# Performance work log

Hardware: AMD Instinct MI355X
Metric: run time of the kernel (lower is better)

Reference implementation:

```python
import jax, jax.numpy as jnp
import numpy as np

N = 100000      # nodes
E = 1600000     # directed edges (before self loops)
IN_DIM = 5
HID = 64
NEG_SLOPE = 0.2  # PyG GATConv default LeakyReLU slope


def setup_inputs() -> dict:
    key = jax.random.key(0)
    ks = jax.random.split(key, 12)
    x = jax.random.normal(ks[0], (N, IN_DIM), dtype=jnp.float32)
    edge_index = jax.random.randint(ks[1], (2, E), 0, N, dtype=jnp.int64)
    # layer 1 params (GATConv(5, HID), heads=1)
    W1 = jax.random.normal(ks[2], (IN_DIM, HID), dtype=jnp.float32) * (1.0 / np.sqrt(IN_DIM))
    a_src1 = jax.random.normal(ks[3], (HID,), dtype=jnp.float32) * 0.1
    a_dst1 = jax.random.normal(ks[4], (HID,), dtype=jnp.float32) * 0.1
    b1 = jnp.zeros((HID,), dtype=jnp.float32)
    # layer 2 params (GATConv(HID, 1))
    W2 = jax.random.normal(ks[5], (HID, 1), dtype=jnp.float32) * (1.0 / np.sqrt(HID))
    a_src2 = jax.random.normal(ks[6], (1,), dtype=jnp.float32) * 0.1
    a_dst2 = jax.random.normal(ks[7], (1,), dtype=jnp.float32) * 0.1
    b2 = jnp.zeros((1,), dtype=jnp.float32)
    return {"x": x, "edge_index": edge_index,
            "W1": W1, "a_src1": a_src1, "a_dst1": a_dst1, "b1": b1,
            "W2": W2, "a_src2": a_src2, "a_dst2": a_dst2, "b2": b2}


def _gat_layer(x, W, a_src, a_dst, b, src, dst):
    h = x @ W                                   # [N, F]
    s_src = h @ a_src                           # [N] per-node src score
    s_dst = h @ a_dst                           # [N] per-node dst score
    e = s_src[src] + s_dst[dst]                 # [E'] edge logits
    e = jnp.where(e > 0, e, NEG_SLOPE * e)      # LeakyReLU(0.2)
    # segment softmax over incoming edges of each dst node
    m = jax.ops.segment_max(e, dst, num_segments=N)
    ex = jnp.exp(e - m[dst])
    denom = jax.ops.segment_sum(ex, dst, num_segments=N)
    coef = ex / denom[dst]                      # [E'] attention coefficients
    out = jax.ops.segment_sum(coef[:, None] * h[src], dst, num_segments=N)
    return out + b


def reference(x, edge_index, W1, a_src1, a_dst1, b1, W2, a_src2, a_dst2, b2):
    si = jnp.arange(N, dtype=edge_index.dtype)  # add self loops (PyG default)
    src = jnp.concatenate([edge_index[0], si])
    dst = jnp.concatenate([edge_index[1], si])
    h = _gat_layer(x, W1, a_src1, a_dst1, b1, src, dst)
    h = jax.nn.relu(h)
    return _gat_layer(h, W2, a_src2, a_dst2, b2, src, dst)  # [N, 1]
```

## Files before the change

### kernel.cpp

```cpp
#include <hip/hip_runtime.h>
#include <hip/hip_bf16.h>
#include <hip/hip_fp16.h>

#define NN 100000
#define EE 1600000
#define ET (EE + NN)
#define HID 64
#define NEG 0.2f
#define NBUK 391
#define SCT_TILE 8192
#define BUKCAP 8192

__device__ __forceinline__ float uh(unsigned u) {
    __half_raw r; r.x = (unsigned short)(u & 0xFFFF);
    return __half2float(__half(r));
}
__device__ __forceinline__ unsigned f2h(float f) {
    __half h = __float2half_rn(f);
    __half_raw r = *reinterpret_cast<__half_raw*>(&h);
    return (unsigned)r.x;
}

#define NSCT ((ET + SCT_TILE - 1) / SCT_TILE)
#define NPROJB ((NN + 31) / 32)

__global__ __launch_bounds__(1024) void k_front(const float* __restrict__ x,
                                                const float* __restrict__ W1,
                                                const float* __restrict__ a_src1,
                                                const float* __restrict__ a_dst1,
                                                const int* __restrict__ ei,
                                                unsigned* __restrict__ rec,
                                                float* __restrict__ sd1,
                                                int* __restrict__ bcur,
                                                unsigned* __restrict__ pairs) {
    __shared__ unsigned sp[SCT_TILE];
    __shared__ unsigned short bid[SCT_TILE];
    __shared__ int cnt_[NBUK], loc[NBUK], cur[NBUK];
    __shared__ int wsum[16];
    int tid = threadIdx.x;

    if (blockIdx.x >= NSCT) {
        int p = blockIdx.x - NSCT;
        int wid  = tid >> 6;
        int half = (tid >> 5) & 1, li = tid & 31;
        int n = p * 32 + wid * 2 + half;
        if (n >= NN) return;
        float xv[5];
        float h0 = 0.f, h1 = 0.f;
#pragma unroll
        for (int k = 0; k < 5; ++k) {
            xv[k] = x[n * 5 + k];
            h0 += xv[k] * W1[k * HID + li];
            h1 += xv[k] * W1[k * HID + li + 32];
        }
        float a = h0 * a_src1[li] + h1 * a_src1[li + 32];
        float b = h0 * a_dst1[li] + h1 * a_dst1[li + 32];
#pragma unroll
        for (int o = 1; o <= 16; o <<= 1) { a += __shfl_xor(a, o); b += __shfl_xor(b, o); }
        if (li == 0) {
            sd1[n] = b;
            uint4 rv;
            rv.x = __float_as_uint(a);
            rv.y = f2h(xv[0]) | (f2h(xv[1]) << 16);
            rv.z = f2h(xv[2]) | (f2h(xv[3]) << 16);
            rv.w = f2h(xv[4]);
            *(uint4*)(rec + (size_t)n * 4) = rv;
        }
        return;
    }

    int wid = tid >> 6, lane = tid & 63;
    int base = blockIdx.x * SCT_TILE;
    int tilecnt = ET - base; if (tilecnt > SCT_TILE) tilecnt = SCT_TILE;

    for (int i = tid; i < NBUK; i += 1024) cnt_[i] = 0;
    __syncthreads();
    int sreg[8], dreg[8], rreg[8];
#pragma unroll
    for (int it = 0; it < 2; ++it) {
        int i = base + (it * 1024 + tid) * 4;
        if (i + 3 < EE) {
            const int4 sv = *(const int4*)(ei + i);
            const int4 dv = *(const int4*)(ei + EE + i);
            sreg[it*4+0] = sv.x; sreg[it*4+1] = sv.y; sreg[it*4+2] = sv.z; sreg[it*4+3] = sv.w;
            dreg[it*4+0] = dv.x; dreg[it*4+1] = dv.y; dreg[it*4+2] = dv.z; dreg[it*4+3] = dv.w;
        } else {
#pragma unroll
            for (int k = 0; k < 4; ++k) {
                int idx = i + k;
                if (idx < EE)      { sreg[it*4+k] = ei[idx];  dreg[it*4+k] = ei[EE + idx]; }
                else if (idx < ET) { sreg[it*4+k] = idx - EE; dreg[it*4+k] = idx - EE; }
                else               { dreg[it*4+k] = -1; }
            }
        }
#pragma unroll
        for (int k = 0; k < 4; ++k)
            if (dreg[it*4+k] >= 0) rreg[it*4+k] = atomicAdd(&cnt_[dreg[it*4+k] >> 8], 1);
    }
    __syncthreads();
    int b0 = tid * 4;
    int s0 = 0;
    if (b0 < NBUK)
        for (int k = 0; k < 4 && b0 + k < NBUK; ++k) s0 += cnt_[b0 + k];
    int incl = s0;
#pragma unroll
    for (int o = 1; o < 64; o <<= 1) {
        int t = __shfl(incl, (lane - o) & 63);
        if (lane >= o) incl += t;
    }
    if (lane == 63) wsum[wid] = incl;
    __syncthreads();
    int wpref = 0;
    for (int w = 0; w < wid; ++w) wpref += wsum[w];
    if (b0 < NBUK) {
        int run = wpref + incl - s0;
        for (int k = 0; k < 4 && b0 + k < NBUK; ++k) {
            loc[b0 + k] = run;
            run += cnt_[b0 + k];
        }
    }
    __syncthreads();
    for (int i = tid; i < NBUK; i += 1024) {
        int c = cnt_[i];
        cur[i] = c ? (atomicAdd(&bcur[i], c) + i * BUKCAP - loc[i]) : 0;
    }
    __syncthreads();
#pragma unroll
    for (int q = 0; q < 8; ++q) {
        if (dreg[q] >= 0) {
            int s = sreg[q], d = dreg[q];
            int b = d >> 8;
            int slot = loc[b] + rreg[q];
            sp[slot]  = ((unsigned)(d & 255) << 17) | (unsigned)s;
            bid[slot] = (unsigned short)b;
        }
    }
    __syncthreads();
    for (int i = tid; i < tilecnt; i += 1024)
        pairs[cur[bid[i]] + i] = sp[i];
}

__global__ __launch_bounds__(1024) void k_bsort(const int* __restrict__ bcur,
                                                unsigned* __restrict__ pairs,
                                                int2* __restrict__ rowcnt) {
    __shared__ int hist[256], sc[256];
    int b = blockIdx.x;
    int cnt = bcur[b];
    if (cnt > BUKCAP) cnt = BUKCAP;
    int base = b * BUKCAP;
    int tid = threadIdx.x;
    if (tid < 256) hist[tid] = 0;
    __syncthreads();
    unsigned preg[8];
    int rreg[8];
    int i0 = tid * 8;
    if (i0 + 8 <= cnt) {
        const uint4 v0 = *(const uint4*)(pairs + base + i0);
        const uint4 v1 = *(const uint4*)(pairs + base + i0 + 4);
        preg[0] = v0.x; preg[1] = v0.y; preg[2] = v0.z; preg[3] = v0.w;
        preg[4] = v1.x; preg[5] = v1.y; preg[6] = v1.z; preg[7] = v1.w;
    } else {
#pragma unroll
        for (int j = 0; j < 8; ++j)
            preg[j] = (i0 + j < cnt) ? pairs[base + i0 + j] : 0xFFFFFFFFu;
    }
#pragma unroll
    for (int j = 0; j < 8; ++j)
        if (preg[j] != 0xFFFFFFFFu) rreg[j] = atomicAdd(&hist[preg[j] >> 17], 1);
    __syncthreads();
    if (tid < 64) {
        int v0 = hist[4 * tid], v1 = hist[4 * tid + 1];
        int v2 = hist[4 * tid + 2], v3 = hist[4 * tid + 3];
        int s = v0 + v1 + v2 + v3;
#pragma unroll
        for (int o = 1; o < 64; o <<= 1) {
            int t = __shfl(s, (tid - o) & 63);
            if (tid >= o) s += t;
        }
        int excl = s - v0 - v1 - v2 - v3;
        sc[4 * tid]     = excl;
        sc[4 * tid + 1] = excl + v0;
        sc[4 * tid + 2] = excl + v0 + v1;
        sc[4 * tid + 3] = excl + v0 + v1 + v2;
    }
    __syncthreads();
    int nbase = b << 8;
    if (tid < 256 && nbase + tid < NN)
        rowcnt[nbase + tid] = make_int2(base + sc[tid], hist[tid]);
    int* adj = (int*)pairs;
#pragma unroll
    for (int j = 0; j < 8; ++j) {
        if (preg[j] != 0xFFFFFFFFu) {
            int ld = (int)(preg[j] >> 17);
            adj[base + sc[ld] + rreg[j]] = (int)(preg[j] & 0x1FFFF);
        }
    }
}

__device__ __forceinline__ void agg1_node_gen(int n, int lane, int off, int deg,
                                              const int* __restrict__ adj,
                                              const unsigned* __restrict__ rec,
                                              const float* __restrict__ sd1,
                                              const float* __restrict__ W1,
                                              const float* __restrict__ b1,
                                              const float* __restrict__ W2,
                                              float* __restrict__ h2) {
    float sdn = sd1[n];
    float dsum = 0.f, a0 = 0.f, a1 = 0.f, a2 = 0.f, a3 = 0.f, a4 = 0.f;
    for (int j0 = 0; j0 < deg; j0 += 64) {
        int j = j0 + lane;
        if (j < deg) {
            int s = adj[off + j];
            const uint4 v = *(const uint4*)(rec + (size_t)s * 4);
            float t = __uint_as_float(v.x) + sdn;
            float e = t > 0.f ? t : NEG * t;
            float w = __expf(e);
            dsum += w;
            a0 += w * uh(v.y); a1 += w * uh(v.y >> 16);
            a2 += w * uh(v.z); a3 += w * uh(v.z >> 16);
            a4 += w * uh(v.w);
        }
    }
#pragma unroll
    for (int o = 32; o; o >>= 1) {
        dsum += __shfl_xor(dsum, o);
        a0 += __shfl_xor(a0, o); a1 += __shfl_xor(a1, o); a2 += __shfl_xor(a2, o);
        a3 += __shfl_xor(a3, o); a4 += __shfl_xor(a4, o);
    }
    float inv = 1.0f / dsum;
    a0 *= inv; a1 *= inv; a2 *= inv; a3 *= inv; a4 *= inv;
    float of = b1[lane] + a0 * W1[lane] + a1 * W1[64 + lane] + a2 * W1[128 + lane]
             + a3 * W1[192 + lane] + a4 * W1[256 + lane];
    of = fmaxf(of, 0.f);
    float p2 = of * W2[lane];
#pragma unroll
    for (int o = 32; o; o >>= 1) p2 += __shfl_xor(p2, o);
    if (lane == 0) h2[n] = p2;
}

__global__ __launch_bounds__(256) void k_agg1(const int* __restrict__ rowcnt,
                                              const int* __restrict__ adj,
                                              const unsigned* __restrict__ rec,
                                              const float* __restrict__ sd1,
                                              const float* __restrict__ W1,
                                              const float* __restrict__ b1,
                                              const float* __restrict__ W2,
                                              float* __restrict__ h2) {
    int wid  = threadIdx.x >> 6;
    int lane = threadIdx.x & 63;
    int n0 = (blockIdx.x * 4 + wid) * 2;
    if (n0 >= NN) return;
    const int4 rc = *(const int4*)(rowcnt + n0 * 2);
    int off0 = rc.x, d0 = rc.y, off1 = rc.z, d1 = rc.w;

    if (d0 <= 32 && d1 <= 32) {
        int half = lane >> 5, li = lane & 31;
        int n = n0 + half;
        int off = half ? off1 : off0;
        int deg = half ? d1 : d0;
        float sdn = sd1[n];
        int s = adj[off + (li < deg ? li : 0)];
        const uint4 v = *(const uint4*)(rec + (size_t)s * 4);
        float t = __uint_as_float(v.x) + sdn;
        float e = t > 0.f ? t : NEG * t;
        float p = (li < deg) ? __expf(e) : 0.f;
        float ds = p;
        float a0 = p * uh(v.y), a1 = p * uh(v.y >> 16);
        float a2 = p * uh(v.z), a3 = p * uh(v.z >> 16);
        float a4 = p * uh(v.w);
#pragma unroll
        for (int o = 1; o <= 16; o <<= 1) {
            ds += __shfl_xor(ds, o);
            a0 += __shfl_xor(a0, o); a1 += __shfl_xor(a1, o); a2 += __shfl_xor(a2, o);
            a3 += __shfl_xor(a3, o); a4 += __shfl_xor(a4, o);
        }
        float inv = 1.0f / ds;
        a0 *= inv; a1 *= inv; a2 *= inv; a3 *= inv; a4 *= inv;
        float o0 = b1[li] + a0 * W1[li] + a1 * W1[64 + li] + a2 * W1[128 + li]
                 + a3 * W1[192 + li] + a4 * W1[256 + li];
        float o1 = b1[li + 32] + a0 * W1[li + 32] + a1 * W1[96 + li] + a2 * W1[160 + li]
                 + a3 * W1[224 + li] + a4 * W1[288 + li];
        o0 = fmaxf(o0, 0.f);
        o1 = fmaxf(o1, 0.f);
        float p2 = o0 * W2[li] + o1 * W2[li + 32];
#pragma unroll
        for (int o = 1; o <= 16; o <<= 1) p2 += __shfl_xor(p2, o);
        if (li == 0) h2[n] = p2;
    } else {
        agg1_node_gen(n0,     lane, off0, d0, adj, rec, sd1, W1, b1, W2, h2);
        agg1_node_gen(n0 + 1, lane, off1, d1, adj, rec, sd1, W1, b1, W2, h2);
    }
}

__device__ __forceinline__ void agg2_node(int n, int lane, int off, int deg,
                                          const int* __restrict__ adj,
                                          const float* __restrict__ h2,
                                          float as2v, float ad2v, float b2v,
                                          float* __restrict__ out) {
    float sdn = h2[n] * ad2v;
    float dsum = 0.f, nsum = 0.f;
    for (int j0 = 0; j0 < deg; j0 += 64) {
        int j = j0 + lane;
        if (j < deg) {
            int s = adj[off + j];
            float hv = h2[s];
            float e = hv * as2v + sdn;
            e = e > 0.f ? e : NEG * e;
            float ex = __expf(e);
            dsum += ex;
            nsum += ex * hv;
        }
    }
#pragma unroll
    for (int o = 32; o; o >>= 1) { dsum += __shfl_xor(dsum, o); nsum += __shfl_xor(nsum, o); }
    if (lane == 0) out[n] = nsum / dsum + b2v;
}

__global__ __launch_bounds__(256) void k_agg2(const int* __restrict__ rowcnt,
                                              const int* __restrict__ adj,
                                              const float* __restrict__ h2,
                                              const float* __restrict__ as2,
                                              const float* __restrict__ ad2,
                                              const float* __restrict__ b2,
                                              float* __restrict__ out) {
    int wid  = threadIdx.x >> 6;
    int lane = threadIdx.x & 63;
    int n0 = (blockIdx.x * 4 + wid) * 4;
    if (n0 >= NN) return;
    float as2v = as2[0], ad2v = ad2[0], b2v = b2[0];
    const int4 rcA = *(const int4*)(rowcnt + n0 * 2);
    const int4 rcB = *(const int4*)(rowcnt + n0 * 2 + 4);
    int d0 = rcA.y, d1 = rcA.w, d2 = rcB.y, d3 = rcB.w;

    if (d0 <= 32 && d1 <= 32 && d2 <= 32 && d3 <= 32) {
        int half = lane >> 5, li = lane & 31;
        int nA = n0 + half, nB = n0 + 2 + half;
        int offA = half ? rcA.z : rcA.x;
        int offB = half ? rcB.z : rcB.x;
        int degA = half ? d1 : d0, degB = half ? d3 : d2;
        float sdA = h2[nA] * ad2v, sdB = h2[nB] * ad2v;
        float hvA = 0.f, hvB = 0.f, pA = 0.f, pB = 0.f;
        if (li < degA) {
            hvA = h2[adj[offA + li]];
            float t = hvA * as2v + sdA;
            pA = __expf(t > 0.f ? t : NEG * t);
        }
        if (li < degB) {
            hvB = h2[adj[offB + li]];
            float t = hvB * as2v + sdB;
            pB = __expf(t > 0.f ? t : NEG * t);
        }
        float dsA = pA, dsB = pB, nsA = pA * hvA, nsB = pB * hvB;
#pragma unroll
        for (int o = 1; o <= 16; o <<= 1) {
            dsA += __shfl_xor(dsA, o); nsA += __shfl_xor(nsA, o);
            dsB += __shfl_xor(dsB, o); nsB += __shfl_xor(nsB, o);
        }
        if (li == 0) {
            out[nA] = nsA / dsA + b2v;
            out[nB] = nsB / dsB + b2v;
        }
    } else {
        agg2_node(n0,     lane, rcA.x, d0, adj, h2, as2v, ad2v, b2v, out);
        agg2_node(n0 + 1, lane, rcA.z, d1, adj, h2, as2v, ad2v, b2v, out);
        agg2_node(n0 + 2, lane, rcB.x, d2, adj, h2, as2v, ad2v, b2v, out);
        agg2_node(n0 + 3, lane, rcB.z, d3, adj, h2, as2v, ad2v, b2v, out);
    }
}

extern "C" void kernel_launch(void* const* d_in, const int* in_sizes, int n_in,
                              void* d_out, int out_size, void* d_ws, size_t ws_size,
                              hipStream_t stream) {
    const float* x      = (const float*)d_in[0];
    const int*   ei     = (const int*)d_in[1];
    const float* W1     = (const float*)d_in[2];
    const float* a_src1 = (const float*)d_in[3];
    const float* a_dst1 = (const float*)d_in[4];
    const float* b1     = (const float*)d_in[5];
    const float* W2     = (const float*)d_in[6];
    const float* as2    = (const float*)d_in[7];
    const float* ad2    = (const float*)d_in[8];
    const float* b2     = (const float*)d_in[9];
    float* out = (float*)d_out;

    unsigned* rec = (unsigned*)d_ws;
    float* sd1  = (float*)(rec + (size_t)NN * 4);
    float* h2   = sd1 + NN;
    int2* rowcnt = (int2*)(h2 + NN);
    int* bcur   = (int*)(rowcnt + NN);
    unsigned* pairs = (unsigned*)(bcur + 1024);
    int* adj    = (int*)pairs;

    const int NPAIR = (NN / 2 + 3) / 4;
    const int NQUAD = (NN + 15) / 16;

    hipMemsetAsync(bcur, 0, 1024 * sizeof(int), stream);
    k_front<<<NSCT + NPROJB, 1024, 0, stream>>>(x, W1, a_src1, a_dst1, ei,
                                                rec, sd1, bcur, pairs);
    k_bsort<<<NBUK, 1024, 0, stream>>>(bcur, pairs, rowcnt);
    k_agg1<<<NPAIR, 256, 0, stream>>>((const int*)rowcnt, adj, rec, sd1, W1, b1, W2, h2);
    k_agg2<<<NQUAD, 256, 0, stream>>>((const int*)rowcnt, adj, h2, as2, ad2, b2, out);
}
```

Before: 76.30 us.

## Fuse all GAT stages into one cooperative persistent kernel with grid syncs

Replaces the memset plus four kernel launches with a single cooperative persistent kernel. Blocks loop over work quanta for scatter and projection, bucket sort, layer-1 aggregation and layer-2 aggregation, separated by grid.sync. It also changes the bucket sort to stage the sorted adjacency in LDS and write it back contiguously. This targets launch gaps and inter-kernel drain at the cost of grid-wide barriers and a grid capped at 512 blocks of 1024 threads. The old multi-kernel path is kept as a fallback.

```diff
diff --git a/kernel.cpp b/kernel.cpp
--- a/kernel.cpp
+++ b/kernel.cpp
@@ -1,6 +1,9 @@
 #include <hip/hip_runtime.h>
 #include <hip/hip_bf16.h>
 #include <hip/hip_fp16.h>
+#include <hip/hip_cooperative_groups.h>
+
+namespace cg = cooperative_groups;
 
 #define NN 100000
 #define EE 1600000
@@ -10,6 +13,11 @@
 #define NBUK 391
 #define SCT_TILE 8192
 #define BUKCAP 8192
+#define TPB 1024
+#define NSCT ((ET + SCT_TILE - 1) / SCT_TILE)
+#define NPROJQ ((NN + 31) / 32)
+#define NAGG1Q ((NN + 31) / 32)
+#define NAGG2Q ((NN + 63) / 64)
 
 __device__ __forceinline__ float uh(unsigned u) {
     __half_raw r; r.x = (unsigned short)(u & 0xFFFF);
@@ -21,64 +29,20 @@
     return (unsigned)r.x;
 }
 
-#define NSCT ((ET + SCT_TILE - 1) / SCT_TILE)
-#define NPROJB ((NN + 31) / 32)
-
-__global__ __launch_bounds__(1024) void k_front(const float* __restrict__ x,
-                                                const float* __restrict__ W1,
-                                                const float* __restrict__ a_src1,
-                                                const float* __restrict__ a_dst1,
-                                                const int* __restrict__ ei,
-                                                unsigned* __restrict__ rec,
-                                                float* __restrict__ sd1,
-                                                int* __restrict__ bcur,
-                                                unsigned* __restrict__ pairs) {
-    __shared__ unsigned sp[SCT_TILE];
-    __shared__ unsigned short bid[SCT_TILE];
-    __shared__ int cnt_[NBUK], loc[NBUK], cur[NBUK];
-    __shared__ int wsum[16];
-    int tid = threadIdx.x;
-
-    if (blockIdx.x >= NSCT) {
-        int p = blockIdx.x - NSCT;
-        int wid  = tid >> 6;
-        int half = (tid >> 5) & 1, li = tid & 31;
-        int n = p * 32 + wid * 2 + half;
-        if (n >= NN) return;
-        float xv[5];
-        float h0 = 0.f, h1 = 0.f;
-#pragma unroll
-        for (int k = 0; k < 5; ++k) {
-            xv[k] = x[n * 5 + k];
-            h0 += xv[k] * W1[k * HID + li];
-            h1 += xv[k] * W1[k * HID + li + 32];
-        }
-        float a = h0 * a_src1[li] + h1 * a_src1[li + 32];
-        float b = h0 * a_dst1[li] + h1 * a_dst1[li + 32];
-#pragma unroll
-        for (int o = 1; o <= 16; o <<= 1) { a += __shfl_xor(a, o); b += __shfl_xor(b, o); }
-        if (li == 0) {
-            sd1[n] = b;
-            uint4 rv;
-            rv.x = __float_as_uint(a);
-            rv.y = f2h(xv[0]) | (f2h(xv[1]) << 16);
-            rv.z = f2h(xv[2]) | (f2h(xv[3]) << 16);
-            rv.w = f2h(xv[4]);
-            *(uint4*)(rec + (size_t)n * 4) = rv;
-        }
-        return;
-    }
-
-    int wid = tid >> 6, lane = tid & 63;
-    int base = blockIdx.x * SCT_TILE;
+
+template <typename SC>
+__device__ __forceinline__ void scatter_tile(SC& sc, int q, int tid, int wid, int lane,
+                                             const int* __restrict__ ei,
+                                             int* __restrict__ bcur,
+                                             unsigned* __restrict__ pairs) {
+    int base = q * SCT_TILE;
     int tilecnt = ET - base; if (tilecnt > SCT_TILE) tilecnt = SCT_TILE;
-
-    for (int i = tid; i < NBUK; i += 1024) cnt_[i] = 0;
+    for (int i = tid; i < NBUK; i += TPB) sc.cnt_[i] = 0;
     __syncthreads();
     int sreg[8], dreg[8], rreg[8];
 #pragma unroll
     for (int it = 0; it < 2; ++it) {
-        int i = base + (it * 1024 + tid) * 4;
+        int i = base + (it * TPB + tid) * 4;
         if (i + 3 < EE) {
             const int4 sv = *(const int4*)(ei + i);
             const int4 dv = *(const int4*)(ei + EE + i);
@@ -95,61 +59,94 @@
         }
 #pragma unroll
         for (int k = 0; k < 4; ++k)
-            if (dreg[it*4+k] >= 0) rreg[it*4+k] = atomicAdd(&cnt_[dreg[it*4+k] >> 8], 1);
+            if (dreg[it*4+k] >= 0) rreg[it*4+k] = atomicAdd(&sc.cnt_[dreg[it*4+k] >> 8], 1);
     }
     __syncthreads();
     int b0 = tid * 4;
     int s0 = 0;
     if (b0 < NBUK)
-        for (int k = 0; k < 4 && b0 + k < NBUK; ++k) s0 += cnt_[b0 + k];
+        for (int k = 0; k < 4 && b0 + k < NBUK; ++k) s0 += sc.cnt_[b0 + k];
     int incl = s0;
 #pragma unroll
     for (int o = 1; o < 64; o <<= 1) {
         int t = __shfl(incl, (lane - o) & 63);
         if (lane >= o) incl += t;
     }
-    if (lane == 63) wsum[wid] = incl;
+    if (lane == 63) sc.wsum[wid] = incl;
     __syncthreads();
     int wpref = 0;
-    for (int w = 0; w < wid; ++w) wpref += wsum[w];
+    for (int w = 0; w < wid; ++w) wpref += sc.wsum[w];
     if (b0 < NBUK) {
         int run = wpref + incl - s0;
         for (int k = 0; k < 4 && b0 + k < NBUK; ++k) {
-            loc[b0 + k] = run;
-            run += cnt_[b0 + k];
-        }
-    }
-    __syncthreads();
-    for (int i = tid; i < NBUK; i += 1024) {
-        int c = cnt_[i];
-        cur[i] = c ? (atomicAdd(&bcur[i], c) + i * BUKCAP - loc[i]) : 0;
-    }
-    __syncthreads();
-#pragma unroll
-    for (int q = 0; q < 8; ++q) {
-        if (dreg[q] >= 0) {
-            int s = sreg[q], d = dreg[q];
+            sc.loc[b0 + k] = run;
+            run += sc.cnt_[b0 + k];
+        }
+    }
+    __syncthreads();
+    for (int i = tid; i < NBUK; i += TPB) {
+        int c = sc.cnt_[i];
+        sc.cur[i] = c ? (atomicAdd(&bcur[i], c) + i * BUKCAP - sc.loc[i]) : 0;
+    }
+    __syncthreads();
+#pragma unroll
+    for (int p = 0; p < 8; ++p) {
+        if (dreg[p] >= 0) {
+            int s = sreg[p], d = dreg[p];
             int b = d >> 8;
-            int slot = loc[b] + rreg[q];
-            sp[slot]  = ((unsigned)(d & 255) << 17) | (unsigned)s;
-            bid[slot] = (unsigned short)b;
-        }
-    }
-    __syncthreads();
-    for (int i = tid; i < tilecnt; i += 1024)
-        pairs[cur[bid[i]] + i] = sp[i];
-}
-
-__global__ __launch_bounds__(1024) void k_bsort(const int* __restrict__ bcur,
-                                                unsigned* __restrict__ pairs,
-                                                int2* __restrict__ rowcnt) {
-    __shared__ int hist[256], sc[256];
-    int b = blockIdx.x;
+            int slot = sc.loc[b] + rreg[p];
+            sc.sp[slot]  = ((unsigned)(d & 255) << 17) | (unsigned)s;
+            sc.bid[slot] = (unsigned short)b;
+        }
+    }
+    __syncthreads();
+    for (int i = tid; i < tilecnt; i += TPB)
+        pairs[sc.cur[sc.bid[i]] + i] = sc.sp[i];
+    __syncthreads();
+}
+
+__device__ __forceinline__ void proj_quantum(int p, int tid, int wid,
+                                             const float* __restrict__ x,
+                                             const float* __restrict__ W1,
+                                             const float* __restrict__ a_src1,
+                                             const float* __restrict__ a_dst1,
+                                             unsigned* __restrict__ rec,
+                                             float* __restrict__ sd1) {
+    int half = (tid >> 5) & 1, li = tid & 31;
+    int n = p * 32 + wid * 2 + half;
+    if (n >= NN) return;
+    float xv[5];
+    float h0 = 0.f, h1 = 0.f;
+#pragma unroll
+    for (int k = 0; k < 5; ++k) {
+        xv[k] = x[n * 5 + k];
+        h0 += xv[k] * W1[k * HID + li];
+        h1 += xv[k] * W1[k * HID + li + 32];
+    }
+    float a = h0 * a_src1[li] + h1 * a_src1[li + 32];
+    float b = h0 * a_dst1[li] + h1 * a_dst1[li + 32];
+#pragma unroll
+    for (int o = 1; o <= 16; o <<= 1) { a += __shfl_xor(a, o); b += __shfl_xor(b, o); }
+    if (li == 0) {
+        sd1[n] = b;
+        uint4 rv;
+        rv.x = __float_as_uint(a);
+        rv.y = f2h(xv[0]) | (f2h(xv[1]) << 16);
+        rv.z = f2h(xv[2]) | (f2h(xv[3]) << 16);
+        rv.w = f2h(xv[4]);
+        *(uint4*)(rec + (size_t)n * 4) = rv;
+    }
+}
+
+template <typename BS>
+__device__ __forceinline__ void bsort_bucket(BS& bs, int b, int tid,
+                                             const int* __restrict__ bcur,
+                                             unsigned* __restrict__ pairs,
+                                             int2* __restrict__ rowcnt) {
     int cnt = bcur[b];
     if (cnt > BUKCAP) cnt = BUKCAP;
     int base = b * BUKCAP;
-    int tid = threadIdx.x;
-    if (tid < 256) hist[tid] = 0;
+    if (tid < 256) bs.hist[tid] = 0;
     __syncthreads();
     unsigned preg[8];
     int rreg[8];
@@ -166,11 +163,11 @@
     }
 #pragma unroll
     for (int j = 0; j < 8; ++j)
-        if (preg[j] != 0xFFFFFFFFu) rreg[j] = atomicAdd(&hist[preg[j] >> 17], 1);
+        if (preg[j] != 0xFFFFFFFFu) rreg[j] = atomicAdd(&bs.hist[preg[j] >> 17], 1);
     __syncthreads();
     if (tid < 64) {
-        int v0 = hist[4 * tid], v1 = hist[4 * tid + 1];
-        int v2 = hist[4 * tid + 2], v3 = hist[4 * tid + 3];
+        int v0 = bs.hist[4 * tid], v1 = bs.hist[4 * tid + 1];
+        int v2 = bs.hist[4 * tid + 2], v3 = bs.hist[4 * tid + 3];
         int s = v0 + v1 + v2 + v3;
 #pragma unroll
         for (int o = 1; o < 64; o <<= 1) {
@@ -178,81 +175,38 @@
             if (tid >= o) s += t;
         }
         int excl = s - v0 - v1 - v2 - v3;
-        sc[4 * tid]     = excl;
-        sc[4 * tid + 1] = excl + v0;
-        sc[4 * tid + 2] = excl + v0 + v1;
-        sc[4 * tid + 3] = excl + v0 + v1 + v2;
+        bs.scn[4 * tid]     = excl;
+        bs.scn[4 * tid + 1] = excl + v0;
+        bs.scn[4 * tid + 2] = excl + v0 + v1;
+        bs.scn[4 * tid + 3] = excl + v0 + v1 + v2;
     }
     __syncthreads();
     int nbase = b << 8;
     if (tid < 256 && nbase + tid < NN)
-        rowcnt[nbase + tid] = make_int2(base + sc[tid], hist[tid]);
-    int* adj = (int*)pairs;
+        rowcnt[nbase + tid] = make_int2(base + bs.scn[tid], bs.hist[tid]);
 #pragma unroll
     for (int j = 0; j < 8; ++j) {
         if (preg[j] != 0xFFFFFFFFu) {
             int ld = (int)(preg[j] >> 17);
-            adj[base + sc[ld] + rreg[j]] = (int)(preg[j] & 0x1FFFF);
-        }
-    }
-}
-
-__device__ __forceinline__ void agg1_node_gen(int n, int lane, int off, int deg,
-                                              const int* __restrict__ adj,
-                                              const unsigned* __restrict__ rec,
-                                              const float* __restrict__ sd1,
-                                              const float* __restrict__ W1,
-                                              const float* __restrict__ b1,
-                                              const float* __restrict__ W2,
-                                              float* __restrict__ h2) {
-    float sdn = sd1[n];
-    float dsum = 0.f, a0 = 0.f, a1 = 0.f, a2 = 0.f, a3 = 0.f, a4 = 0.f;
-    for (int j0 = 0; j0 < deg; j0 += 64) {
-        int j = j0 + lane;
-        if (j < deg) {
-            int s = adj[off + j];
-            const uint4 v = *(const uint4*)(rec + (size_t)s * 4);
-            float t = __uint_as_float(v.x) + sdn;
-            float e = t > 0.f ? t : NEG * t;
-            float w = __expf(e);
-            dsum += w;
-            a0 += w * uh(v.y); a1 += w * uh(v.y >> 16);
-            a2 += w * uh(v.z); a3 += w * uh(v.z >> 16);
-            a4 += w * uh(v.w);
-        }
-    }
-#pragma unroll
-    for (int o = 32; o; o >>= 1) {
-        dsum += __shfl_xor(dsum, o);
-        a0 += __shfl_xor(a0, o); a1 += __shfl_xor(a1, o); a2 += __shfl_xor(a2, o);
-        a3 += __shfl_xor(a3, o); a4 += __shfl_xor(a4, o);
-    }
-    float inv = 1.0f / dsum;
-    a0 *= inv; a1 *= inv; a2 *= inv; a3 *= inv; a4 *= inv;
-    float of = b1[lane] + a0 * W1[lane] + a1 * W1[64 + lane] + a2 * W1[128 + lane]
-             + a3 * W1[192 + lane] + a4 * W1[256 + lane];
-    of = fmaxf(of, 0.f);
-    float p2 = of * W2[lane];
-#pragma unroll
-    for (int o = 32; o; o >>= 1) p2 += __shfl_xor(p2, o);
-    if (lane == 0) h2[n] = p2;
-}
-
-__global__ __launch_bounds__(256) void k_agg1(const int* __restrict__ rowcnt,
-                                              const int* __restrict__ adj,
-                                              const unsigned* __restrict__ rec,
-                                              const float* __restrict__ sd1,
-                                              const float* __restrict__ W1,
-                                              const float* __restrict__ b1,
-                                              const float* __restrict__ W2,
-                                              float* __restrict__ h2) {
-    int wid  = threadIdx.x >> 6;
-    int lane = threadIdx.x & 63;
-    int n0 = (blockIdx.x * 4 + wid) * 2;
-    if (n0 >= NN) return;
-    const int4 rc = *(const int4*)(rowcnt + n0 * 2);
+            bs.srt[bs.scn[ld] + rreg[j]] = (int)(preg[j] & 0x1FFFF);
+        }
+    }
+    __syncthreads();
+    int* adj = (int*)pairs;
+    for (int i = tid; i < cnt; i += TPB)
+        adj[base + i] = bs.srt[i];
+    __syncthreads();
+}
+
+__device__ __forceinline__ void agg1_pair(int n0, int lane, const int4 rc,
+                                          const int* __restrict__ adj,
+                                          const unsigned* __restrict__ rec,
+                                          const float* __restrict__ sd1,
+                                          const float* __restrict__ W1,
+                                          const float* __restrict__ b1,
+                                          const float* __restrict__ W2,
+                                          float* __restrict__ h2) {
     int off0 = rc.x, d0 = rc.y, off1 = rc.z, d1 = rc.w;
-
     if (d0 <= 32 && d1 <= 32) {
         int half = lane >> 5, li = lane & 31;
         int n = n0 + half;
@@ -287,51 +241,51 @@
         for (int o = 1; o <= 16; o <<= 1) p2 += __shfl_xor(p2, o);
         if (li == 0) h2[n] = p2;
     } else {
-        agg1_node_gen(n0,     lane, off0, d0, adj, rec, sd1, W1, b1, W2, h2);
-        agg1_node_gen(n0 + 1, lane, off1, d1, adj, rec, sd1, W1, b1, W2, h2);
-    }
-}
-
-__device__ __forceinline__ void agg2_node(int n, int lane, int off, int deg,
+        for (int w = 0; w < 2; ++w) {
+            int n = n0 + w;
+            int off = w ? rc.z : rc.x;
+            int deg = w ? rc.w : rc.y;
+            float sdn = sd1[n];
+            float dsum = 0.f, a0 = 0.f, a1 = 0.f, a2 = 0.f, a3 = 0.f, a4 = 0.f;
+            for (int j0 = 0; j0 < deg; j0 += 64) {
+                int j = j0 + lane;
+                if (j < deg) {
+                    int s = adj[off + j];
+                    const uint4 v = *(const uint4*)(rec + (size_t)s * 4);
+                    float t = __uint_as_float(v.x) + sdn;
+                    float e = t > 0.f ? t : NEG * t;
+                    float ww = __expf(e);
+                    dsum += ww;
+                    a0 += ww * uh(v.y); a1 += ww * uh(v.y >> 16);
+                    a2 += ww * uh(v.z); a3 += ww * uh(v.z >> 16);
+                    a4 += ww * uh(v.w);
+                }
+            }
+#pragma unroll
+            for (int o = 32; o; o >>= 1) {
+                dsum += __shfl_xor(dsum, o);
+                a0 += __shfl_xor(a0, o); a1 += __shfl_xor(a1, o); a2 += __shfl_xor(a2, o);
+                a3 += __shfl_xor(a3, o); a4 += __shfl_xor(a4, o);
+            }
+            float inv = 1.0f / dsum;
+            a0 *= inv; a1 *= inv; a2 *= inv; a3 *= inv; a4 *= inv;
+            float of = b1[lane] + a0 * W1[lane] + a1 * W1[64 + lane] + a2 * W1[128 + lane]
+                     + a3 * W1[192 + lane] + a4 * W1[256 + lane];
+            of = fmaxf(of, 0.f);
+            float p2 = of * W2[lane];
+#pragma unroll
+            for (int o = 32; o; o >>= 1) p2 += __shfl_xor(p2, o);
+            if (lane == 0) h2[n] = p2;
+        }
+    }
+}
+
+__device__ __forceinline__ void agg2_quad(int n0, int lane, const int4 rcA, const int4 rcB,
                                           const int* __restrict__ adj,
                                           const float* __restrict__ h2,
                                           float as2v, float ad2v, float b2v,
                                           float* __restrict__ out) {
-    float sdn = h2[n] * ad2v;
-    float dsum = 0.f, nsum = 0.f;
-    for (int j0 = 0; j0 < deg; j0 += 64) {
-        int j = j0 + lane;
-        if (j < deg) {
-            int s = adj[off + j];
-            float hv = h2[s];
-            float e = hv * as2v + sdn;
-            e = e > 0.f ? e : NEG * e;
-            float ex = __expf(e);
-            dsum += ex;
-            nsum += ex * hv;
-        }
-    }
-#pragma unroll
-    for (int o = 32; o; o >>= 1) { dsum += __shfl_xor(dsum, o); nsum += __shfl_xor(nsum, o); }
-    if (lane == 0) out[n] = nsum / dsum + b2v;
-}
-
-__global__ __launch_bounds__(256) void k_agg2(const int* __restrict__ rowcnt,
-                                              const int* __restrict__ adj,
-                                              const float* __restrict__ h2,
-                                              const float* __restrict__ as2,
-                                              const float* __restrict__ ad2,
-                                              const float* __restrict__ b2,
-                                              float* __restrict__ out) {
-    int wid  = threadIdx.x >> 6;
-    int lane = threadIdx.x & 63;
-    int n0 = (blockIdx.x * 4 + wid) * 4;
-    if (n0 >= NN) return;
-    float as2v = as2[0], ad2v = ad2[0], b2v = b2[0];
-    const int4 rcA = *(const int4*)(rowcnt + n0 * 2);
-    const int4 rcB = *(const int4*)(rowcnt + n0 * 2 + 4);
     int d0 = rcA.y, d1 = rcA.w, d2 = rcB.y, d3 = rcB.w;
-
     if (d0 <= 32 && d1 <= 32 && d2 <= 32 && d3 <= 32) {
         int half = lane >> 5, li = lane & 31;
         int nA = n0 + half, nB = n0 + 2 + half;
@@ -361,11 +315,159 @@
             out[nB] = nsB / dsB + b2v;
         }
     } else {
-        agg2_node(n0,     lane, rcA.x, d0, adj, h2, as2v, ad2v, b2v, out);
-        agg2_node(n0 + 1, lane, rcA.z, d1, adj, h2, as2v, ad2v, b2v, out);
-        agg2_node(n0 + 2, lane, rcB.x, d2, adj, h2, as2v, ad2v, b2v, out);
-        agg2_node(n0 + 3, lane, rcB.z, d3, adj, h2, as2v, ad2v, b2v, out);
-    }
+        for (int w = 0; w < 4; ++w) {
+            int n = n0 + w;
+            int off = (w == 0) ? rcA.x : (w == 1) ? rcA.z : (w == 2) ? rcB.x : rcB.z;
+            int deg = (w == 0) ? d0 : (w == 1) ? d1 : (w == 2) ? d2 : d3;
+            float sdn = h2[n] * ad2v;
+            float dsum = 0.f, nsum = 0.f;
+            for (int j0 = 0; j0 < deg; j0 += 64) {
+                int j = j0 + lane;
+                if (j < deg) {
+                    int s = adj[off + j];
+                    float hv = h2[s];
+                    float e = hv * as2v + sdn;
+                    e = e > 0.f ? e : NEG * e;
+                    float ex = __expf(e);
+                    dsum += ex;
+                    nsum += ex * hv;
+                }
+            }
+#pragma unroll
+            for (int o = 32; o; o >>= 1) { dsum += __shfl_xor(dsum, o); nsum += __shfl_xor(nsum, o); }
+            if (lane == 0) out[n] = nsum / dsum + b2v;
+        }
+    }
+}
+
+struct ScatterLDS {
+    unsigned sp[SCT_TILE];
+    unsigned short bid[SCT_TILE];
+    int cnt_[NBUK], loc[NBUK], cur[NBUK];
+    int wsum[16];
+};
+struct BsortLDS {
+    int srt[BUKCAP];
+    int hist[256], scn[256];
+};
+
+__global__ __launch_bounds__(TPB, 2) void k_mega(const float* __restrict__ x,
+                                                 const float* __restrict__ W1,
+                                                 const float* __restrict__ a_src1,
+                                                 const float* __restrict__ a_dst1,
+                                                 const int* __restrict__ ei,
+                                                 const float* __restrict__ b1,
+                                                 const float* __restrict__ W2,
+                                                 const float* __restrict__ as2,
+                                                 const float* __restrict__ ad2,
+                                                 const float* __restrict__ b2,
+                                                 unsigned* __restrict__ rec,
+                                                 float* __restrict__ sd1,
+                                                 int* __restrict__ bcur,
+                                                 unsigned* __restrict__ pairs,
+                                                 int2* __restrict__ rowcnt,
+                                                 float* __restrict__ h2,
+                                                 float* __restrict__ out) {
+    cg::grid_group grid = cg::this_grid();
+    __shared__ union { ScatterLDS sc; BsortLDS bs; } sh;
+    int tid = threadIdx.x;
+    int wid = tid >> 6, lane = tid & 63;
+    int bx = blockIdx.x;
+    int GS = gridDim.x;
+    int* adj = (int*)pairs;
+
+    for (int i = bx * TPB + tid; i < 1024; i += GS * TPB) bcur[i] = 0;
+    grid.sync();
+
+    for (int q = bx; q < NSCT + NPROJQ; q += GS) {
+        if (q < NSCT)
+            scatter_tile(sh.sc, q, tid, wid, lane, ei, bcur, pairs);
+        else
+            proj_quantum(q - NSCT, tid, wid, x, W1, a_src1, a_dst1, rec, sd1);
+    }
+    grid.sync();
+
+    for (int b = bx; b < NBUK; b += GS)
+        bsort_bucket(sh.bs, b, tid, bcur, pairs, rowcnt);
+    grid.sync();
+
+    const int* rc32 = (const int*)rowcnt;
+    for (int q = bx; q < NAGG1Q; q += GS) {
+        int n0 = q * 32 + wid * 2;
+        if (n0 >= NN) continue;
+        const int4 rc = *(const int4*)(rc32 + n0 * 2);
+        agg1_pair(n0, lane, rc, adj, rec, sd1, W1, b1, W2, h2);
+    }
+    grid.sync();
+
+    float as2v = as2[0], ad2v = ad2[0], b2v = b2[0];
+    for (int q = bx; q < NAGG2Q; q += GS) {
+        int n0 = q * 64 + wid * 4;
+        if (n0 >= NN) continue;
+        const int4 rcA = *(const int4*)(rc32 + n0 * 2);
+        const int4 rcB = *(const int4*)(rc32 + n0 * 2 + 4);
+        agg2_quad(n0, lane, rcA, rcB, adj, h2, as2v, ad2v, b2v, out);
+    }
+}
+
+#define NPROJB ((NN + 31) / 32)
+
+__global__ __launch_bounds__(TPB) void f_front(const float* __restrict__ x,
+                                               const float* __restrict__ W1,
+                                               const float* __restrict__ a_src1,
+                                               const float* __restrict__ a_dst1,
+                                               const int* __restrict__ ei,
+                                               unsigned* __restrict__ rec,
+                                               float* __restrict__ sd1,
+                                               int* __restrict__ bcur,
+                                               unsigned* __restrict__ pairs) {
+    __shared__ ScatterLDS sc;
+    int tid = threadIdx.x;
+    int wid = tid >> 6, lane = tid & 63;
+    if (blockIdx.x >= NSCT) {
+        proj_quantum(blockIdx.x - NSCT, tid, wid, x, W1, a_src1, a_dst1, rec, sd1);
+        return;
+    }
+    scatter_tile(sc, blockIdx.x, tid, wid, lane, ei, bcur, pairs);
+}
+
+__global__ __launch_bounds__(TPB) void f_bsort(const int* __restrict__ bcur,
+                                               unsigned* __restrict__ pairs,
+                                               int2* __restrict__ rowcnt) {
+    __shared__ BsortLDS bs;
+    bsort_bucket(bs, blockIdx.x, threadIdx.x, bcur, pairs, rowcnt);
+}
+
+__global__ __launch_bounds__(256) void f_agg1(const int* __restrict__ rowcnt,
+                                              const int* __restrict__ adj,
+                                              const unsigned* __restrict__ rec,
+                                              const float* __restrict__ sd1,
+                                              const float* __restrict__ W1,
+                                              const float* __restrict__ b1,
+                                              const float* __restrict__ W2,
+                                              float* __restrict__ h2) {
+    int wid  = threadIdx.x >> 6;
+    int lane = threadIdx.x & 63;
+    int n0 = (blockIdx.x * 4 + wid) * 2;
+    if (n0 >= NN) return;
+    const int4 rc = *(const int4*)(rowcnt + n0 * 2);
+    agg1_pair(n0, lane, rc, adj, rec, sd1, W1, b1, W2, h2);
+}
+
+__global__ __launch_bounds__(256) void f_agg2(const int* __restrict__ rowcnt,
+                                              const int* __restrict__ adj,
+                                              const float* __restrict__ h2,
+                                              const float* __restrict__ as2,
+                                              const float* __restrict__ ad2,
+                                              const float* __restrict__ b2,
+                                              float* __restrict__ out) {
+    int wid  = threadIdx.x >> 6;
+    int lane = threadIdx.x & 63;
+    int n0 = (blockIdx.x * 4 + wid) * 4;
+    if (n0 >= NN) return;
+    const int4 rcA = *(const int4*)(rowcnt + n0 * 2);
+    const int4 rcB = *(const int4*)(rowcnt + n0 * 2 + 4);
+    agg2_quad(n0, lane, rcA, rcB, adj, h2, as2[0], ad2[0], b2[0], out);
 }
 
 extern "C" void kernel_launch(void* const* d_in, const int* in_sizes, int n_in,
@@ -391,13 +493,38 @@
     unsigned* pairs = (unsigned*)(bcur + 1024);
     int* adj    = (int*)pairs;
 
-    const int NPAIR = (NN / 2 + 3) / 4;
-    const int NQUAD = (NN + 15) / 16;
-
-    hipMemsetAsync(bcur, 0, 1024 * sizeof(int), stream);
-    k_front<<<NSCT + NPROJB, 1024, 0, stream>>>(x, W1, a_src1, a_dst1, ei,
-                                                rec, sd1, bcur, pairs);
-    k_bsort<<<NBUK, 1024, 0, stream>>>(bcur, pairs, rowcnt);
-    k_agg1<<<NPAIR, 256, 0, stream>>>((const int*)rowcnt, adj, rec, sd1, W1, b1, W2, h2);
-    k_agg2<<<NQUAD, 256, 0, stream>>>((const int*)rowcnt, adj, h2, as2, ad2, b2, out);
-}
+    bool done = false;
+    int dev = 0;
+    if (hipGetDevice(&dev) == hipSuccess) {
+        int coop = 0, ncu = 0, maxB = 0;
+        hipDeviceGetAttribute(&coop, hipDeviceAttributeCooperativeLaunch, dev);
+        hipDeviceGetAttribute(&ncu, hipDeviceAttributeMultiprocessorCount, dev);
+        hipError_t oe = hipOccupancyMaxActiveBlocksPerMultiprocessor(
+                            &maxB, (const void*)k_mega, TPB, 0);
+        if (coop && oe == hipSuccess && maxB > 0 && ncu > 0) {
+            int g = maxB * ncu;
+            if (g > 512) g = 512;
+            void* args[] = {
+                (void*)&x, (void*)&W1, (void*)&a_src1, (void*)&a_dst1, (void*)&ei,
+                (void*)&b1, (void*)&W2, (void*)&as2, (void*)&ad2, (void*)&b2,
+                (void*)&rec, (void*)&sd1, (void*)&bcur, (void*)&pairs, (void*)&rowcnt,
+                (void*)&h2, (void*)&out
+            };
+            hipError_t le = hipLaunchCooperativeKernel((const void*)k_mega, dim3(g),
+                                                       dim3(TPB), args, 0, stream);
+            if (le == hipSuccess) done = true;
+            else (void)hipGetLastError();
+        }
+    }
+
+    if (!done) {
+        const int NPAIR = (NN / 2 + 3) / 4;
+        const int NQUAD = (NN + 15) / 16;
+        hipMemsetAsync(bcur, 0, 1024 * sizeof(int), stream);
+        f_front<<<NSCT + NPROJB, TPB, 0, stream>>>(x, W1, a_src1, a_dst1, ei,
+                                                   rec, sd1, bcur, pairs);
+        f_bsort<<<NBUK, TPB, 0, stream>>>(bcur, pairs, rowcnt);
+        f_agg1<<<NPAIR, 256, 0, stream>>>((const int*)rowcnt, adj, rec, sd1, W1, b1, W2, h2);
+        f_agg2<<<NQUAD, 256, 0, stream>>>((const int*)rowcnt, adj, h2, as2, ad2, b2, out);
+    }
+}
```

New measurement: 70.56 us. 1.08x faster.
